# Kernel tuning notes

Hardware: AMD Instinct MI355X
Metric: run time of the kernel (lower is better)

## Reference

```python
import jax, jax.numpy as jnp
import numpy as np

N_ITER = 100
EPS = 1e-12


def _corr(x, k):
    # x: [C,H,W], k: [kh,kw]; per-channel 'same' cross-correlation, zero padding
    C = x.shape[0]
    kern = jnp.broadcast_to(k, (C, 1) + k.shape)
    return jax.lax.conv_general_dilated(
        x[None], kern, window_strides=(1, 1), padding='SAME',
        feature_group_count=C,
        dimension_numbers=('NCHW', 'OIHW', 'NCHW'))[0]


def _corr_t(x, k):
    # adjoint of zero-padded 'same' correlation = correlation with flipped kernel
    return _corr(x, k[::-1, ::-1])


def _A(x, kernel, reg_kernels, w2):
    # A x = K^T K x + sum_i w_i^2 R_i^T R_i x
    out = _corr_t(_corr(x, kernel), kernel)
    for i in range(reg_kernels.shape[0]):  # small fixed number of reg kernels
        rk = reg_kernels[i]
        out = out + w2[i] * _corr_t(_corr(x, rk), rk)
    return out


def setup_inputs() -> dict:
    key = jax.random.key(0)
    k1, k2, k3, k4 = jax.random.split(key, 4)
    image = jax.random.uniform(k1, (3, 768, 768), dtype=jnp.float32)
    kernel = jax.random.uniform(k2, (15, 15), dtype=jnp.float32)
    kernel = kernel / jnp.sum(kernel)  # normalized blur PSF
    reg_kernels = jax.random.normal(k3, (2, 5, 5), dtype=jnp.float32)
    reg_kernel_weights = jax.random.uniform(
        k4, (2,), dtype=jnp.float32, minval=1e-6, maxval=1.0)
    return {'image': image, 'kernel': kernel, 'reg_kernels': reg_kernels,
            'reg_kernel_weights': reg_kernel_weights}


def reference(image, kernel, reg_kernels, reg_kernel_weights):
    w2 = reg_kernel_weights ** 2
    # CG init: x0 = image, b = image, solve A x = K^T b
    KTb = _corr_t(image, kernel)
    r0 = KTb - _A(image, kernel, reg_kernels, w2)
    xrp0 = jnp.stack([image, r0, r0])  # [3, C, H, W]: x, r, p

    def body(xrp, _):
        x, r, p = xrp[0], xrp[1], xrp[2]
        Ap = _A(p, kernel, reg_kernels, w2)
        rtr = jnp.sum(r * r, axis=(1, 2), keepdims=True)      # per-channel [C,1,1]
        ptAp = jnp.sum(p * Ap, axis=(1, 2), keepdims=True)
        alpha = rtr / (ptAp + EPS)
        x_new = x + alpha * p
        r_new = r - alpha * Ap
        beta = jnp.sum(r_new * r_new, axis=(1, 2), keepdims=True) / (rtr + EPS)
        p_new = r_new + beta * p
        return jnp.stack([x_new, r_new, p_new]), None

    xrp, _ = jax.lax.scan(jax.checkpoint(body), xrp0, None, length=N_ITER)
    return xrp
```

## Files before the change

### kernel.cpp

```cpp
#include <hip/hip_runtime.h>

#define EPS 1e-12f

constexpr int H = 768, W = 768, C = 3;
constexpr int HW = H * W;
constexpr int CHW = C * HW;

constexpr int NSLOT = 16;
constexpr int SSTR = 16;
constexpr int SCALSZ = NSLOT * SSTR;

constexpr int SPW = 100, SPH = 60;
constexpr int S0W = 84;
constexpr int S1W = 76, S1H = 36;
constexpr int UBUF = SPH * SPW;
constexpr int LDSE = UBUF + 2 * S1H * S1W;
constexpr int IPW = 92, IPH = 60;

__device__ __forceinline__ float block_reduce_256(float v, float* redbuf) {
    #pragma unroll
    for (int off = 32; off > 0; off >>= 1) v += __shfl_down(v, off, 64);
    const int tid = threadIdx.x;
    if ((tid & 63) == 0) redbuf[tid >> 6] = v;
    __syncthreads();
    return redbuf[0] + redbuf[1] + redbuf[2] + redbuf[3];
}

__device__ __forceinline__ float sum_slots(const float* base, int c) {
    float s = 0.f;
    #pragma unroll
    for (int k = 0; k < NSLOT; ++k) s += base[k * SSTR + c];
    return s;
}

__global__ void tap_prep_k(const float* __restrict__ k15, const float* __restrict__ rks,
                           const float* __restrict__ rw, float* __restrict__ taps) {
    const int tid = threadIdx.x;
    if (tid < 240) {
        const int i = tid >> 4, j = tid & 15;
        taps[tid]       = (j < 15) ? k15[i * 15 + j] : 0.f;
        taps[240 + tid] = (j < 15) ? k15[(14 - i) * 15 + (14 - j)] : 0.f;
    }
    if (tid < 80) {
        const int kk = tid / 40, rem = tid % 40, i = rem >> 3, j = rem & 7;
        taps[480 + tid] = (j < 5) ? rks[kk * 25 + i * 5 + j] : 0.f;
        taps[560 + tid] = (j < 5) ? rks[kk * 25 + (4 - i) * 5 + (4 - j)] : 0.f;
    }
    const float w20 = rw[0] * rw[0], w21 = rw[1] * rw[1];
    if (tid == 0) { taps[1684] = w20; taps[1685] = w21; }
    for (int t = tid; t < 29 * 36; t += 256) {
        const int uy = t / 36, ux = t - uy * 36;
        float s = 0.f;
        if (ux < 29) {
            const int dy = uy - 14, dx = ux - 14;
            for (int sy = 0; sy < 15; ++sy) {
                const int ty = sy + dy;
                if ((unsigned)ty >= 15u) continue;
                for (int sx = 0; sx < 15; ++sx) {
                    const int tx = sx + dx;
                    if ((unsigned)tx < 15u) s += k15[sy * 15 + sx] * k15[ty * 15 + tx];
                }
            }
            if (dy >= -4 && dy <= 4 && dx >= -4 && dx <= 4) {
                float q0 = 0.f, q1 = 0.f;
                for (int sy = 0; sy < 5; ++sy) {
                    const int ty = sy + dy;
                    if ((unsigned)ty >= 5u) continue;
                    for (int sx = 0; sx < 5; ++sx) {
                        const int tx = sx + dx;
                        if ((unsigned)tx >= 5u) continue;
                        q0 += rks[sy * 5 + sx] * rks[ty * 5 + tx];
                        q1 += rks[25 + sy * 5 + sx] * rks[25 + ty * 5 + tx];
                    }
                }
                s += w20 * q0 + w21 * q1;
            }
        }
        taps[640 + t] = s;
    }
}

__global__ __launch_bounds__(256) void prologue_k(
    const float* __restrict__ img, const float* __restrict__ taps,
    float* __restrict__ outR, float* __restrict__ outP, float* __restrict__ outX,
    float* __restrict__ red)
{
    __shared__ __align__(16) float ub[UBUF];
    __shared__ __align__(16) float st1[S1H * S1W];
    __shared__ __align__(16) float st2[S1H * S1W];
    __shared__ float redbuf[4];

    const float* kt   = taps;
    const float* ktf  = taps + 240;
    const float* rkt  = taps + 480;
    const float* rktf = taps + 560;
    const float w02 = taps[1684], w12 = taps[1685];

    const int c = blockIdx.z;
    const int bx = blockIdx.x * 64, by = blockIdx.y * 32;
    const int tid = threadIdx.x;
    const float* inC = img + c * HW;

    for (int t = tid; t < SPH * 96; t += 256) {
        const int ly = t / 96, lx = t - ly * 96;
        const int gy = by - 14 + ly, gx = bx - 14 + lx;
        float v = 0.f;
        if ((unsigned)gy < (unsigned)H && (unsigned)gx < (unsigned)W) v = inC[gy * W + gx];
        ub[ly * SPW + lx] = v;
    }
    __syncthreads();

    const int oy = tid >> 3;
    const int ox = (tid & 7) << 3;

    {
        const int s0 = tid, s1i = tid + 256;
        const int row0 = s0 / 9, c0 = (s0 - row0 * 9) << 3;
        const int row1 = s1i / 9, c1 = (s1i - row1 * 9) << 3;
        const bool v1 = (s1i < 324);
        float b0[8], c0a[8], b1[8], c1a[8];
        #pragma unroll
        for (int k = 0; k < 8; ++k) { b0[k] = 0.f; c0a[k] = 0.f; b1[k] = 0.f; c1a[k] = 0.f; }
        #pragma unroll 1
        for (int i = 0; i < 5; ++i) {
            float kb[8], kc[8];
            #pragma unroll
            for (int q = 0; q < 2; ++q) {
                *(float4*)(kb + 4 * q) = *(const float4*)(rkt + i * 8 + 4 * q);
                *(float4*)(kc + 4 * q) = *(const float4*)(rkt + 40 + i * 8 + 4 * q);
            }
            {
                const float* rp = ub + (row0 + 10 + i) * SPW + c0 + 8;
                float seg[16];
                #pragma unroll
                for (int q = 0; q < 4; ++q) *(float4*)(seg + 4 * q) = *(const float4*)(rp + 4 * q);
                #pragma unroll
                for (int j = 0; j < 5; ++j)
                    #pragma unroll
                    for (int k = 0; k < 8; ++k) {
                        b0[k]  = fmaf(seg[j + k + 2], kb[j], b0[k]);
                        c0a[k] = fmaf(seg[j + k + 2], kc[j], c0a[k]);
                    }
            }
            if (v1) {
                const float* rp = ub + (row1 + 10 + i) * SPW + c1 + 8;
                float seg[16];
                #pragma unroll
                for (int q = 0; q < 4; ++q) *(float4*)(seg + 4 * q) = *(const float4*)(rp + 4 * q);
                #pragma unroll
                for (int j = 0; j < 5; ++j)
                    #pragma unroll
                    for (int k = 0; k < 8; ++k) {
                        b1[k]  = fmaf(seg[j + k + 2], kb[j], b1[k]);
                        c1a[k] = fmaf(seg[j + k + 2], kc[j], c1a[k]);
                    }
            }
        }
        {
            const int gy = by - 2 + row0, gxb = bx - 2 + c0;
            #pragma unroll
            for (int k = 0; k < 8; ++k)
                if (((unsigned)gy >= (unsigned)H) || ((unsigned)(gxb + k) >= (unsigned)W)) { b0[k] = 0.f; c0a[k] = 0.f; }
            float* o1 = st1 + row0 * S1W + c0;
            float* o2 = st2 + row0 * S1W + c0;
            *(float4*)(o1) = make_float4(b0[0], b0[1], b0[2], b0[3]);
            *(float4*)(o1 + 4) = make_float4(b0[4], b0[5], b0[6], b0[7]);
            *(float4*)(o2) = make_float4(c0a[0], c0a[1], c0a[2], c0a[3]);
            *(float4*)(o2 + 4) = make_float4(c0a[4], c0a[5], c0a[6], c0a[7]);
        }
        if (v1) {
            const int gy = by - 2 + row1, gxb = bx - 2 + c1;
            #pragma unroll
            for (int k = 0; k < 8; ++k)
                if (((unsigned)gy >= (unsigned)H) || ((unsigned)(gxb + k) >= (unsigned)W)) { b1[k] = 0.f; c1a[k] = 0.f; }
            float* o1 = st1 + row1 * S1W + c1;
            float* o2 = st2 + row1 * S1W + c1;
            *(float4*)(o1) = make_float4(b1[0], b1[1], b1[2], b1[3]);
            *(float4*)(o1 + 4) = make_float4(b1[4], b1[5], b1[6], b1[7]);
            *(float4*)(o2) = make_float4(c1a[0], c1a[1], c1a[2], c1a[3]);
            *(float4*)(o2 + 4) = make_float4(c1a[4], c1a[5], c1a[6], c1a[7]);
        }
    }

    float pctr[8];
    {
        const float* ctr = ub + (oy + 14) * SPW + ox + 14;
        #pragma unroll
        for (int k = 0; k < 8; ++k) pctr[k] = ctr[k];
    }

    float vimg[8];
    #pragma unroll
    for (int k = 0; k < 8; ++k) vimg[k] = 0.f;
    #pragma unroll 1
    for (int i = 0; i < 15; ++i) {
        const float* rowp = ub + (oy + 7 + i) * SPW + ox + 4;
        float seg[28];
        #pragma unroll
        for (int q = 0; q < 7; ++q) *(float4*)(seg + 4 * q) = *(const float4*)(rowp + 4 * q);
        float kv[16];
        #pragma unroll
        for (int q = 0; q < 4; ++q) *(float4*)(kv + 4 * q) = *(const float4*)(ktf + i * 16 + 4 * q);
        #pragma unroll
        for (int j = 0; j < 15; ++j)
            #pragma unroll
            for (int k = 0; k < 8; ++k) vimg[k] = fmaf(seg[j + k + 3], kv[j], vimg[k]);
    }

    const int s0 = tid, s1i = tid + 256;
    const int row0 = s0 / 10, ca0 = (s0 - row0 * 10) << 3;
    const int row1 = s1i / 10, ca1 = (s1i - row1 * 10) << 3;
    const bool av1 = (s1i < 460);
    float a0[8], a1[8];
    #pragma unroll
    for (int k = 0; k < 8; ++k) { a0[k] = 0.f; a1[k] = 0.f; }
    #pragma unroll 1
    for (int i = 0; i < 15; ++i) {
        float kv[16];
        #pragma unroll
        for (int q = 0; q < 4; ++q) *(float4*)(kv + 4 * q) = *(const float4*)(kt + i * 16 + 4 * q);
        {
            const float* rp = ub + (row0 + i) * SPW + ca0;
            float seg[24];
            #pragma unroll
            for (int q = 0; q < 6; ++q) *(float4*)(seg + 4 * q) = *(const float4*)(rp + 4 * q);
            #pragma unroll
            for (int j = 0; j < 15; ++j)
                #pragma unroll
                for (int k = 0; k < 8; ++k) a0[k] = fmaf(seg[j + k], kv[j], a0[k]);
        }
        if (av1) {
            const float* rp = ub + (row1 + i) * SPW + ca1;
            float seg[24];
            #pragma unroll
            for (int q = 0; q < 6; ++q) *(float4*)(seg + 4 * q) = *(const float4*)(rp + 4 * q);
            #pragma unroll
            for (int j = 0; j < 15; ++j)
                #pragma unroll
                for (int k = 0; k < 8; ++k) a1[k] = fmaf(seg[j + k], kv[j], a1[k]);
        }
    }
    {
        const int gy = by - 7 + row0, gxb = bx - 7 + ca0;
        #pragma unroll
        for (int k = 0; k < 8; ++k)
            if (((unsigned)gy >= (unsigned)H) || ((unsigned)(gxb + k) >= (unsigned)W)) a0[k] = 0.f;
    }
    if (av1) {
        const int gy = by - 7 + row1, gxb = bx - 7 + ca1;
        #pragma unroll
        for (int k = 0; k < 8; ++k)
            if (((unsigned)gy >= (unsigned)H) || ((unsigned)(gxb + k) >= (unsigned)W)) a1[k] = 0.f;
    }
    __syncthreads();
    {
        float* o = ub + row0 * S0W + ca0;
        *(float4*)(o) = make_float4(a0[0], a0[1], a0[2], a0[3]);
        *(float4*)(o + 4) = make_float4(a0[4], a0[5], a0[6], a0[7]);
    }
    if (av1) {
        float* o = ub + row1 * S0W + ca1;
        *(float4*)(o) = make_float4(a1[0], a1[1], a1[2], a1[3]);
        *(float4*)(o + 4) = make_float4(a1[4], a1[5], a1[6], a1[7]);
    }
    __syncthreads();

    float acc[8];
    #pragma unroll
    for (int k = 0; k < 8; ++k) acc[k] = 0.f;
    #pragma unroll 1
    for (int i = 0; i < 15; ++i) {
        float kv[16];
        #pragma unroll
        for (int q = 0; q < 4; ++q) *(float4*)(kv + 4 * q) = *(const float4*)(ktf + i * 16 + 4 * q);
        const float* rp = ub + (oy + i) * S0W + ox;
        float seg[24];
        #pragma unroll
        for (int q = 0; q < 6; ++q) *(float4*)(seg + 4 * q) = *(const float4*)(rp + 4 * q);
        #pragma unroll
        for (int j = 0; j < 15; ++j)
            #pragma unroll
            for (int k = 0; k < 8; ++k) acc[k] = fmaf(seg[j + k], kv[j], acc[k]);
    }
    float accB[8], accC[8];
    #pragma unroll
    for (int k = 0; k < 8; ++k) { accB[k] = 0.f; accC[k] = 0.f; }
    #pragma unroll 1
    for (int i = 0; i < 5; ++i) {
        float kb[8], kc[8];
        #pragma unroll
        for (int q = 0; q < 2; ++q) {
            *(float4*)(kb + 4 * q) = *(const float4*)(rktf + i * 8 + 4 * q);
            *(float4*)(kc + 4 * q) = *(const float4*)(rktf + 40 + i * 8 + 4 * q);
        }
        const float* r1p = st1 + (oy + i) * S1W + ox;
        const float* r2p = st2 + (oy + i) * S1W + ox;
        float sA[12], sB[12];
        #pragma unroll
        for (int q = 0; q < 3; ++q) *(float4*)(sA + 4 * q) = *(const float4*)(r1p + 4 * q);
        #pragma unroll
        for (int q = 0; q < 3; ++q) *(float4*)(sB + 4 * q) = *(const float4*)(r2p + 4 * q);
        #pragma unroll
        for (int j = 0; j < 5; ++j)
            #pragma unroll
            for (int k = 0; k < 8; ++k) {
                accB[k] = fmaf(sA[j + k], kb[j], accB[k]);
                accC[k] = fmaf(sB[j + k], kc[j], accC[k]);
            }
    }

    float v[8];
    #pragma unroll
    for (int k = 0; k < 8; ++k) v[k] = vimg[k] - (acc[k] + w02 * accB[k] + w12 * accC[k]);

    const int g = c * HW + (by + oy) * W + bx + ox;
    *(float4*)(outR + g)     = make_float4(v[0], v[1], v[2], v[3]);
    *(float4*)(outR + g + 4) = make_float4(v[4], v[5], v[6], v[7]);
    *(float4*)(outP + g)     = make_float4(v[0], v[1], v[2], v[3]);
    *(float4*)(outP + g + 4) = make_float4(v[4], v[5], v[6], v[7]);
    *(float4*)(outX + g)     = make_float4(pctr[0], pctr[1], pctr[2], pctr[3]);
    *(float4*)(outX + g + 4) = make_float4(pctr[4], pctr[5], pctr[6], pctr[7]);
    float local = 0.f;
    #pragma unroll
    for (int k = 0; k < 8; ++k) local += v[k] * v[k];
    const float tot = block_reduce_256(local, redbuf);
    if (tid == 0) {
        const int bid = blockIdx.y * gridDim.x + blockIdx.x;
        atomicAdd(red + (bid & (NSLOT - 1)) * SSTR + c, tot);
    }
}

template <bool FIRST>
__global__ __launch_bounds__(256) void stepA_k(
    const float* __restrict__ pold, const float* __restrict__ rvec,
    float* __restrict__ x, const float* __restrict__ taps,
    float* __restrict__ Apnew, float* __restrict__ pnew,
    const float* __restrict__ rtrI, const float* __restrict__ rtrIm1,
    const float* __restrict__ ptapIm1, float* __restrict__ ptapI)
{
    __shared__ __align__(16) float lds[LDSE];
    __shared__ float redbuf[4];
    const int c = blockIdx.z;
    const int tid = threadIdx.x;
    const int bid = blockIdx.x;

    float alpha = 0.f, beta = 0.f;
    if (!FIRST) {
        const float ri   = sum_slots(rtrI, c);
        const float rim1 = sum_slots(rtrIm1, c);
        const float ptm1 = sum_slots(ptapIm1, c);
        beta  = ri / (rim1 + EPS);
        alpha = rim1 / (ptm1 + EPS);
    }

    float S1 = 0.f;

    if (bid < 68) {
        float* ub  = lds;
        float* st1 = lds + UBUF;
        float* st2 = st1 + S1H * S1W;
        const float* kt   = taps;
        const float* ktf  = taps + 240;
        const float* rkt  = taps + 480;
        const float* rktf = taps + 560;
        const float w02 = taps[1684], w12 = taps[1685];

        int tbx, tby;
        { const int e = bid;
          if (e < 12)      { tbx = e;      tby = 0; }
          else if (e < 24) { tbx = e - 12; tby = 23; }
          else if (e < 46) { tbx = 0;      tby = 1 + (e - 24); }
          else             { tbx = 11;     tby = 1 + (e - 46); } }
        const int bx = tbx * 64, by = tby * 32;

        for (int s = tid; s < SPH * 96; s += 256) {
            const int ly = s / 96, lx = s - ly * 96;
            const int gy = by - 14 + ly, gx = bx - 14 + lx;
            float pe = 0.f;
            if ((unsigned)gy < (unsigned)H && (unsigned)gx < (unsigned)W) {
                const int g = c * HW + gy * W + gx;
                const float pv = pold[g];
                if (FIRST) pe = pv;
                else {
                    pe = fmaf(beta, pv, rvec[g]);
                    if (ly >= 14 && ly < 46 && lx >= 14 && lx < 78) {
                        pnew[g] = pe;
                        x[g] = fmaf(alpha, pv, x[g]);
                    }
                }
            }
            ub[ly * SPW + lx] = pe;
        }
        __syncthreads();

        const int oy = tid >> 3;
        const int ox = (tid & 7) << 3;

        {
            const int s0 = tid, s1i = tid + 256;
            const int row0 = s0 / 9, c0 = (s0 - row0 * 9) << 3;
            const int row1 = s1i / 9, c1 = (s1i - row1 * 9) << 3;
            const bool v1 = (s1i < 324);
            float b0[8], c0a[8], b1[8], c1a[8];
            #pragma unroll
            for (int k = 0; k < 8; ++k) { b0[k] = 0.f; c0a[k] = 0.f; b1[k] = 0.f; c1a[k] = 0.f; }
            #pragma unroll 1
            for (int i = 0; i < 5; ++i) {
                float kb[8], kc[8];
                #pragma unroll
                for (int q = 0; q < 2; ++q) {
                    *(float4*)(kb + 4 * q) = *(const float4*)(rkt + i * 8 + 4 * q);
                    *(float4*)(kc + 4 * q) = *(const float4*)(rkt + 40 + i * 8 + 4 * q);
                }
                {
                    const float* rp = ub + (row0 + 10 + i) * SPW + c0 + 8;
                    float seg[16];
                    #pragma unroll
                    for (int q = 0; q < 4; ++q) *(float4*)(seg + 4 * q) = *(const float4*)(rp + 4 * q);
                    #pragma unroll
                    for (int j = 0; j < 5; ++j)
                        #pragma unroll
                        for (int k = 0; k < 8; ++k) {
                            b0[k]  = fmaf(seg[j + k + 2], kb[j], b0[k]);
                            c0a[k] = fmaf(seg[j + k + 2], kc[j], c0a[k]);
                        }
                }
                if (v1) {
                    const float* rp = ub + (row1 + 10 + i) * SPW + c1 + 8;
                    float seg[16];
                    #pragma unroll
                    for (int q = 0; q < 4; ++q) *(float4*)(seg + 4 * q) = *(const float4*)(rp + 4 * q);
                    #pragma unroll
                    for (int j = 0; j < 5; ++j)
                        #pragma unroll
                        for (int k = 0; k < 8; ++k) {
                            b1[k]  = fmaf(seg[j + k + 2], kb[j], b1[k]);
                            c1a[k] = fmaf(seg[j + k + 2], kc[j], c1a[k]);
                        }
                }
            }
            {
                const int gy = by - 2 + row0, gxb = bx - 2 + c0;
                #pragma unroll
                for (int k = 0; k < 8; ++k)
                    if (((unsigned)gy >= (unsigned)H) || ((unsigned)(gxb + k) >= (unsigned)W)) { b0[k] = 0.f; c0a[k] = 0.f; }
                float* o1 = st1 + row0 * S1W + c0;
                float* o2 = st2 + row0 * S1W + c0;
                *(float4*)(o1) = make_float4(b0[0], b0[1], b0[2], b0[3]);
                *(float4*)(o1 + 4) = make_float4(b0[4], b0[5], b0[6], b0[7]);
                *(float4*)(o2) = make_float4(c0a[0], c0a[1], c0a[2], c0a[3]);
                *(float4*)(o2 + 4) = make_float4(c0a[4], c0a[5], c0a[6], c0a[7]);
            }
            if (v1) {
                const int gy = by - 2 + row1, gxb = bx - 2 + c1;
                #pragma unroll
                for (int k = 0; k < 8; ++k)
                    if (((unsigned)gy >= (unsigned)H) || ((unsigned)(gxb + k) >= (unsigned)W)) { b1[k] = 0.f; c1a[k] = 0.f; }
                float* o1 = st1 + row1 * S1W + c1;
                float* o2 = st2 + row1 * S1W + c1;
                *(float4*)(o1) = make_float4(b1[0], b1[1], b1[2], b1[3]);
                *(float4*)(o1 + 4) = make_float4(b1[4], b1[5], b1[6], b1[7]);
                *(float4*)(o2) = make_float4(c1a[0], c1a[1], c1a[2], c1a[3]);
                *(float4*)(o2 + 4) = make_float4(c1a[4], c1a[5], c1a[6], c1a[7]);
            }
        }

        float pctr[8];
        {
            const float* ctr = ub + (oy + 14) * SPW + ox + 14;
            #pragma unroll
            for (int k = 0; k < 8; ++k) pctr[k] = ctr[k];
        }

        const int s0 = tid, s1i = tid + 256;
        const int row0 = s0 / 10, ca0 = (s0 - row0 * 10) << 3;
        const int row1 = s1i / 10, ca1 = (s1i - row1 * 10) << 3;
        const bool av1 = (s1i < 460);
        float a0[8], a1[8];
        #pragma unroll
        for (int k = 0; k < 8; ++k) { a0[k] = 0.f; a1[k] = 0.f; }
        #pragma unroll 1
        for (int i = 0; i < 15; ++i) {
            float kv[16];
            #pragma unroll
            for (int q = 0; q < 4; ++q) *(float4*)(kv + 4 * q) = *(const float4*)(kt + i * 16 + 4 * q);
            {
                const float* rp = ub + (row0 + i) * SPW + ca0;
                float seg[24];
                #pragma unroll
                for (int q = 0; q < 6; ++q) *(float4*)(seg + 4 * q) = *(const float4*)(rp + 4 * q);
                #pragma unroll
                for (int j = 0; j < 15; ++j)
                    #pragma unroll
                    for (int k = 0; k < 8; ++k) a0[k] = fmaf(seg[j + k], kv[j], a0[k]);
            }
            if (av1) {
                const float* rp = ub + (row1 + i) * SPW + ca1;
                float seg[24];
                #pragma unroll
                for (int q = 0; q < 6; ++q) *(float4*)(seg + 4 * q) = *(const float4*)(rp + 4 * q);
                #pragma unroll
                for (int j = 0; j < 15; ++j)
                    #pragma unroll
                    for (int k = 0; k < 8; ++k) a1[k] = fmaf(seg[j + k], kv[j], a1[k]);
            }
        }
        {
            const int gy = by - 7 + row0, gxb = bx - 7 + ca0;
            #pragma unroll
            for (int k = 0; k < 8; ++k)
                if (((unsigned)gy >= (unsigned)H) || ((unsigned)(gxb + k) >= (unsigned)W)) a0[k] = 0.f;
        }
        if (av1) {
            const int gy = by - 7 + row1, gxb = bx - 7 + ca1;
            #pragma unroll
            for (int k = 0; k < 8; ++k)
                if (((unsigned)gy >= (unsigned)H) || ((unsigned)(gxb + k) >= (unsigned)W)) a1[k] = 0.f;
        }
        __syncthreads();
        {
            float* o = ub + row0 * S0W + ca0;
            *(float4*)(o) = make_float4(a0[0], a0[1], a0[2], a0[3]);
            *(float4*)(o + 4) = make_float4(a0[4], a0[5], a0[6], a0[7]);
        }
        if (av1) {
            float* o = ub + row1 * S0W + ca1;
            *(float4*)(o) = make_float4(a1[0], a1[1], a1[2], a1[3]);
            *(float4*)(o + 4) = make_float4(a1[4], a1[5], a1[6], a1[7]);
        }
        __syncthreads();

        float acc[8];
        #pragma unroll
        for (int k = 0; k < 8; ++k) acc[k] = 0.f;
        #pragma unroll 1
        for (int i = 0; i < 15; ++i) {
            float kv[16];
            #pragma unroll
            for (int q = 0; q < 4; ++q) *(float4*)(kv + 4 * q) = *(const float4*)(ktf + i * 16 + 4 * q);
            const float* rp = ub + (oy + i) * S0W + ox;
            float seg[24];
            #pragma unroll
            for (int q = 0; q < 6; ++q) *(float4*)(seg + 4 * q) = *(const float4*)(rp + 4 * q);
            #pragma unroll
            for (int j = 0; j < 15; ++j)
                #pragma unroll
                for (int k = 0; k < 8; ++k) acc[k] = fmaf(seg[j + k], kv[j], acc[k]);
        }
        float accB[8], accC[8];
        #pragma unroll
        for (int k = 0; k < 8; ++k) { accB[k] = 0.f; accC[k] = 0.f; }
        #pragma unroll 1
        for (int i = 0; i < 5; ++i) {
            float kb[8], kc[8];
            #pragma unroll
            for (int q = 0; q < 2; ++q) {
                *(float4*)(kb + 4 * q) = *(const float4*)(rktf + i * 8 + 4 * q);
                *(float4*)(kc + 4 * q) = *(const float4*)(rktf + 40 + i * 8 + 4 * q);
            }
            const float* r1p = st1 + (oy + i) * S1W + ox;
            const float* r2p = st2 + (oy + i) * S1W + ox;
            float sA[12], sB[12];
            #pragma unroll
            for (int q = 0; q < 3; ++q) *(float4*)(sA + 4 * q) = *(const float4*)(r1p + 4 * q);
            #pragma unroll
            for (int q = 0; q < 3; ++q) *(float4*)(sB + 4 * q) = *(const float4*)(r2p + 4 * q);
            #pragma unroll
            for (int j = 0; j < 5; ++j)
                #pragma unroll
                for (int k = 0; k < 8; ++k) {
                    accB[k] = fmaf(sA[j + k], kb[j], accB[k]);
                    accC[k] = fmaf(sB[j + k], kc[j], accC[k]);
                }
        }

        float v[8];
        #pragma unroll
        for (int k = 0; k < 8; ++k) v[k] = acc[k] + w02 * accB[k] + w12 * accC[k];

        const int g = c * HW + (by + oy) * W + bx + ox;
        *(float4*)(Apnew + g)     = make_float4(v[0], v[1], v[2], v[3]);
        *(float4*)(Apnew + g + 4) = make_float4(v[4], v[5], v[6], v[7]);
        #pragma unroll
        for (int k = 0; k < 8; ++k) S1 += pctr[k] * v[k];
    } else {
        const float* tk = taps + 640;
        const int b = bid - 68;
        const int bx = 64 + (b % 10) * 64, by = 32 + (b / 10) * 32;
        const int gy0 = by - 14, gx0 = bx - 14;

        for (int s = tid; s < IPH * IPW; s += 256) {
            const int ly = s / IPW, lx = s - ly * IPW;
            const int g = c * HW + (gy0 + ly) * W + (gx0 + lx);
            const float pv = pold[g];
            float pe;
            if (FIRST) pe = pv;
            else {
                pe = fmaf(beta, pv, rvec[g]);
                if (ly >= 14 && ly < 46 && lx >= 14 && lx < 78) {
                    pnew[g] = pe;
                    x[g] = fmaf(alpha, pv, x[g]);
                }
            }
            lds[s] = pe;
        }
        __syncthreads();

        const int ox = (tid & 15) << 2;
        const int o0 = (tid >> 4) << 1;

        float a0[4], a1[4];
        #pragma unroll
        for (int k = 0; k < 4; ++k) { a0[k] = 0.f; a1[k] = 0.f; }
        {
            const float* rp = lds + o0 * IPW + ox;
            float seg[32];
            #pragma unroll
            for (int q = 0; q < 8; ++q) *(float4*)(seg + 4 * q) = *(const float4*)(rp + 4 * q);
            #pragma unroll
            for (int j = 0; j < 29; ++j) {
                const float kv = tk[j];
                #pragma unroll
                for (int k = 0; k < 4; ++k) a0[k] = fmaf(seg[j + k], kv, a0[k]);
            }
        }
        #pragma unroll 1
        for (int d = 1; d <= 28; ++d) {
            const float* rp = lds + (o0 + d) * IPW + ox;
            float seg[32];
            #pragma unroll
            for (int q = 0; q < 8; ++q) *(float4*)(seg + 4 * q) = *(const float4*)(rp + 4 * q);
            const float* kr0 = tk + d * 36;
            const float* kr1 = kr0 - 36;
            #pragma unroll
            for (int j = 0; j < 29; ++j) {
                const float kv0 = kr0[j], kv1 = kr1[j];
                #pragma unroll
                for (int k = 0; k < 4; ++k) {
                    a0[k] = fmaf(seg[j + k], kv0, a0[k]);
                    a1[k] = fmaf(seg[j + k], kv1, a1[k]);
                }
            }
        }
        {
            const float* rp = lds + (o0 + 29) * IPW + ox;
            float seg[32];
            #pragma unroll
            for (int q = 0; q < 8; ++q) *(float4*)(seg + 4 * q) = *(const float4*)(rp + 4 * q);
            const float* kr1 = tk + 28 * 36;
            #pragma unroll
            for (int j = 0; j < 29; ++j) {
                const float kv = kr1[j];
                #pragma unroll
                for (int k = 0; k < 4; ++k) a1[k] = fmaf(seg[j + k], kv, a1[k]);
            }
        }

        const int gbase = c * HW + (by + o0) * W + bx + ox;
        const float* c0p = lds + (o0 + 14) * IPW + ox + 14;
        const float* c1p = c0p + IPW;
        *(float4*)(Apnew + gbase)     = make_float4(a0[0], a0[1], a0[2], a0[3]);
        *(float4*)(Apnew + gbase + W) = make_float4(a1[0], a1[1], a1[2], a1[3]);
        #pragma unroll
        for (int k = 0; k < 4; ++k) S1 += c0p[k] * a0[k] + c1p[k] * a1[k];
    }

    const float tot = block_reduce_256(S1, redbuf);
    if (tid == 0) atomicAdd(ptapI + (bid & (NSLOT - 1)) * SSTR + c, tot);
}

__global__ __launch_bounds__(256) void cgr_k(
    float* __restrict__ r, const float* __restrict__ Ap,
    const float* __restrict__ rtrI, const float* __restrict__ ptapI,
    float* __restrict__ rtrNext)
{
    __shared__ float redbuf[4];
    const int c = blockIdx.z;
    const float alpha = sum_slots(rtrI, c) / (sum_slots(ptapI, c) + EPS);
    const int idx = c * HW + (blockIdx.x * 256 + threadIdx.x) * 8;
    float local = 0.f;
    #pragma unroll
    for (int h = 0; h < 2; ++h) {
        const int o = idx + 4 * h;
        float4 rv = *(float4*)(r + o);
        const float4 av = *(const float4*)(Ap + o);
        rv.x = fmaf(-alpha, av.x, rv.x);
        rv.y = fmaf(-alpha, av.y, rv.y);
        rv.z = fmaf(-alpha, av.z, rv.z);
        rv.w = fmaf(-alpha, av.w, rv.w);
        *(float4*)(r + o) = rv;
        local += rv.x * rv.x + rv.y * rv.y + rv.z * rv.z + rv.w * rv.w;
    }
    const float tot = block_reduce_256(local, redbuf);
    if (threadIdx.x == 0)
        atomicAdd(rtrNext + ((int)blockIdx.x & (NSLOT - 1)) * SSTR + c, tot);
}

__global__ __launch_bounds__(256) void ep_k(
    float* __restrict__ x, const float* __restrict__ r100, const float* __restrict__ p99,
    float* __restrict__ pout,
    const float* __restrict__ rtr99s, const float* __restrict__ rtr100s,
    const float* __restrict__ ptap99s)
{
    const int c = blockIdx.z;
    const float rtr99 = sum_slots(rtr99s, c);
    const float alpha = rtr99 / (sum_slots(ptap99s, c) + EPS);
    const float beta  = sum_slots(rtr100s, c) / (rtr99 + EPS);
    const int idx = c * HW + (blockIdx.x * 256 + threadIdx.x) * 8;
    #pragma unroll
    for (int h = 0; h < 2; ++h) {
        const int o = idx + 4 * h;
        const float4 pv = *(const float4*)(p99 + o);
        const float4 rv = *(const float4*)(r100 + o);
        float4 xv = *(float4*)(x + o);
        xv.x = fmaf(alpha, pv.x, xv.x); xv.y = fmaf(alpha, pv.y, xv.y);
        xv.z = fmaf(alpha, pv.z, xv.z); xv.w = fmaf(alpha, pv.w, xv.w);
        *(float4*)(x + o) = xv;
        *(float4*)(pout + o) = make_float4(
            fmaf(beta, pv.x, rv.x), fmaf(beta, pv.y, rv.y),
            fmaf(beta, pv.z, rv.z), fmaf(beta, pv.w, rv.w));
    }
}

extern "C" void kernel_launch(void* const* d_in, const int* in_sizes, int n_in,
                              void* d_out, int out_size, void* d_ws, size_t ws_size,
                              hipStream_t stream)
{
    const float* img = (const float*)d_in[0];
    const float* k15 = (const float*)d_in[1];
    const float* rks = (const float*)d_in[2];
    const float* rw  = (const float*)d_in[3];

    float* out = (float*)d_out;
    float* xs = out;
    float* rs = out + CHW;
    float* ps = out + 2 * CHW;

    float* ws = (float*)d_ws;
    float* pA   = ws;
    float* pB   = ws + CHW;
    float* Ap   = ws + 2 * CHW;
    float* scal = ws + 3 * CHW;
    float* rtrS  = scal;
    float* ptapS = scal + 101 * SCALSZ;
    float* taps  = scal + 201 * SCALSZ;

    float* pbuf[2] = { pA, pB };

    hipMemsetAsync(scal, 0, (size_t)201 * SCALSZ * sizeof(float), stream);
    tap_prep_k<<<1, 256, 0, stream>>>(k15, rks, rw, taps);

    const dim3 bc(256);
    prologue_k<<<dim3(12, 24, 3), bc, 0, stream>>>(img, taps, rs, pA, xs, rtrS);

    for (int i = 0; i < 100; ++i) {
        if (i == 0) {
            stepA_k<true><<<dim3(288, 1, 3), bc, 0, stream>>>(
                pA, rs, xs, taps, Ap, nullptr,
                rtrS, rtrS, ptapS, ptapS);
        } else {
            stepA_k<false><<<dim3(288, 1, 3), bc, 0, stream>>>(
                pbuf[(i - 1) & 1], rs, xs, taps, Ap, pbuf[i & 1],
                rtrS + (size_t)i * SCALSZ, rtrS + (size_t)(i - 1) * SCALSZ,
                ptapS + (size_t)(i - 1) * SCALSZ, ptapS + (size_t)i * SCALSZ);
        }
        cgr_k<<<dim3(288, 1, 3), bc, 0, stream>>>(
            rs, Ap, rtrS + (size_t)i * SCALSZ, ptapS + (size_t)i * SCALSZ,
            rtrS + (size_t)(i + 1) * SCALSZ);
    }
    ep_k<<<dim3(288, 1, 3), bc, 0, stream>>>(
        xs, rs, pB, ps,
        rtrS + (size_t)99 * SCALSZ, rtrS + (size_t)100 * SCALSZ,
        ptapS + (size_t)99 * SCALSZ);
}
```

Measured before the change: 8.744 ms.

## Split edge tiles into half-height blocks and move x update into residual kernel

Border tiles of the fused A·p kernel are split into two 16-row halves, so there are 136 edge blocks instead of 68, each with a smaller LDS footprint and 4 outputs per thread. This is meant to rebalance the slow padded edge blocks against the interior blocks. The x += alpha·p update moves from stepA (where it ran against the previous p) into cgr_k using the current p, which removes the alpha computation from stepA but adds an extra read and write stream to cgr_k. Splitting the edge tiles also recomputes more halo per block.

```diff
diff --git a/kernel.cpp b/kernel.cpp
--- a/kernel.cpp
+++ b/kernel.cpp
@@ -14,8 +14,13 @@
 constexpr int S0W = 84;
 constexpr int S1W = 76, S1H = 36;
 constexpr int UBUF = SPH * SPW;
-constexpr int LDSE = UBUF + 2 * S1H * S1W;
+
+constexpr int ESPH = 44;
+constexpr int ET0H = 30;
+constexpr int ES1H = 20;
+constexpr int ELDS = ESPH * SPW + 2 * ES1H * S1W;
 constexpr int IPW = 92, IPH = 60;
+constexpr int NEDGE = 136;
 
 __device__ __forceinline__ float block_reduce_256(float v, float* redbuf) {
     #pragma unroll
@@ -333,47 +338,41 @@
 template <bool FIRST>
 __global__ __launch_bounds__(256) void stepA_k(
     const float* __restrict__ pold, const float* __restrict__ rvec,
-    float* __restrict__ x, const float* __restrict__ taps,
+    const float* __restrict__ taps,
     float* __restrict__ Apnew, float* __restrict__ pnew,
     const float* __restrict__ rtrI, const float* __restrict__ rtrIm1,
-    const float* __restrict__ ptapIm1, float* __restrict__ ptapI)
+    float* __restrict__ ptapI)
 {
-    __shared__ __align__(16) float lds[LDSE];
+    __shared__ __align__(16) float lds[ELDS];
     __shared__ float redbuf[4];
     const int c = blockIdx.z;
     const int tid = threadIdx.x;
     const int bid = blockIdx.x;
 
-    float alpha = 0.f, beta = 0.f;
-    if (!FIRST) {
-        const float ri   = sum_slots(rtrI, c);
-        const float rim1 = sum_slots(rtrIm1, c);
-        const float ptm1 = sum_slots(ptapIm1, c);
-        beta  = ri / (rim1 + EPS);
-        alpha = rim1 / (ptm1 + EPS);
-    }
+    float beta = 0.f;
+    if (!FIRST) beta = sum_slots(rtrI, c) / (sum_slots(rtrIm1, c) + EPS);
 
     float S1 = 0.f;
 
-    if (bid < 68) {
+    if (bid < NEDGE) {
         float* ub  = lds;
-        float* st1 = lds + UBUF;
-        float* st2 = st1 + S1H * S1W;
+        float* st1 = lds + ESPH * SPW;
+        float* st2 = st1 + ES1H * S1W;
         const float* kt   = taps;
         const float* ktf  = taps + 240;
         const float* rkt  = taps + 480;
         const float* rktf = taps + 560;
         const float w02 = taps[1684], w12 = taps[1685];
 
+        const int e = bid >> 1, half = bid & 1;
         int tbx, tby;
-        { const int e = bid;
-          if (e < 12)      { tbx = e;      tby = 0; }
+        { if (e < 12)      { tbx = e;      tby = 0; }
           else if (e < 24) { tbx = e - 12; tby = 23; }
           else if (e < 46) { tbx = 0;      tby = 1 + (e - 24); }
           else             { tbx = 11;     tby = 1 + (e - 46); } }
-        const int bx = tbx * 64, by = tby * 32;
-
-        for (int s = tid; s < SPH * 96; s += 256) {
+        const int bx = tbx * 64, by = tby * 32 + half * 16;
+
+        for (int s = tid; s < ESPH * 96; s += 256) {
             const int ly = s / 96, lx = s - ly * 96;
             const int gy = by - 14 + ly, gx = bx - 14 + lx;
             float pe = 0.f;
@@ -383,36 +382,31 @@
                 if (FIRST) pe = pv;
                 else {
                     pe = fmaf(beta, pv, rvec[g]);
-                    if (ly >= 14 && ly < 46 && lx >= 14 && lx < 78) {
-                        pnew[g] = pe;
-                        x[g] = fmaf(alpha, pv, x[g]);
+                    if (ly >= 14 && ly < 30 && lx >= 14 && lx < 78) pnew[g] = pe;
+                }
+            }
+            ub[ly * SPW + lx] = pe;
+        }
+        __syncthreads();
+
+        const int oy2 = tid >> 4;
+        const int ox2 = (tid & 15) << 2;
+
+        {
+            const int row0 = tid / 9, c0 = (tid - (tid / 9) * 9) << 3;
+            const bool act = (tid < 180);
+            float b0[8], c0a[8];
+            #pragma unroll
+            for (int k = 0; k < 8; ++k) { b0[k] = 0.f; c0a[k] = 0.f; }
+            if (act) {
+                #pragma unroll 1
+                for (int i = 0; i < 5; ++i) {
+                    float kb[8], kc[8];
+                    #pragma unroll
+                    for (int q = 0; q < 2; ++q) {
+                        *(float4*)(kb + 4 * q) = *(const float4*)(rkt + i * 8 + 4 * q);
+                        *(float4*)(kc + 4 * q) = *(const float4*)(rkt + 40 + i * 8 + 4 * q);
                     }
-                }
-            }
-            ub[ly * SPW + lx] = pe;
-        }
-        __syncthreads();
-
-        const int oy = tid >> 3;
-        const int ox = (tid & 7) << 3;
-
-        {
-            const int s0 = tid, s1i = tid + 256;
-            const int row0 = s0 / 9, c0 = (s0 - row0 * 9) << 3;
-            const int row1 = s1i / 9, c1 = (s1i - row1 * 9) << 3;
-            const bool v1 = (s1i < 324);
-            float b0[8], c0a[8], b1[8], c1a[8];
-            #pragma unroll
-            for (int k = 0; k < 8; ++k) { b0[k] = 0.f; c0a[k] = 0.f; b1[k] = 0.f; c1a[k] = 0.f; }
-            #pragma unroll 1
-            for (int i = 0; i < 5; ++i) {
-                float kb[8], kc[8];
-                #pragma unroll
-                for (int q = 0; q < 2; ++q) {
-                    *(float4*)(kb + 4 * q) = *(const float4*)(rkt + i * 8 + 4 * q);
-                    *(float4*)(kc + 4 * q) = *(const float4*)(rkt + 40 + i * 8 + 4 * q);
-                }
-                {
                     const float* rp = ub + (row0 + 10 + i) * SPW + c0 + 8;
                     float seg[16];
                     #pragma unroll
@@ -425,21 +419,6 @@
                             c0a[k] = fmaf(seg[j + k + 2], kc[j], c0a[k]);
                         }
                 }
-                if (v1) {
-                    const float* rp = ub + (row1 + 10 + i) * SPW + c1 + 8;
-                    float seg[16];
-                    #pragma unroll
-                    for (int q = 0; q < 4; ++q) *(float4*)(seg + 4 * q) = *(const float4*)(rp + 4 * q);
-                    #pragma unroll
-                    for (int j = 0; j < 5; ++j)
-                        #pragma unroll
-                        for (int k = 0; k < 8; ++k) {
-                            b1[k]  = fmaf(seg[j + k + 2], kb[j], b1[k]);
-                            c1a[k] = fmaf(seg[j + k + 2], kc[j], c1a[k]);
-                        }
-                }
-            }
-            {
                 const int gy = by - 2 + row0, gxb = bx - 2 + c0;
                 #pragma unroll
                 for (int k = 0; k < 8; ++k)
@@ -451,31 +430,19 @@
                 *(float4*)(o2) = make_float4(c0a[0], c0a[1], c0a[2], c0a[3]);
                 *(float4*)(o2 + 4) = make_float4(c0a[4], c0a[5], c0a[6], c0a[7]);
             }
-            if (v1) {
-                const int gy = by - 2 + row1, gxb = bx - 2 + c1;
-                #pragma unroll
-                for (int k = 0; k < 8; ++k)
-                    if (((unsigned)gy >= (unsigned)H) || ((unsigned)(gxb + k) >= (unsigned)W)) { b1[k] = 0.f; c1a[k] = 0.f; }
-                float* o1 = st1 + row1 * S1W + c1;
-                float* o2 = st2 + row1 * S1W + c1;
-                *(float4*)(o1) = make_float4(b1[0], b1[1], b1[2], b1[3]);
-                *(float4*)(o1 + 4) = make_float4(b1[4], b1[5], b1[6], b1[7]);
-                *(float4*)(o2) = make_float4(c1a[0], c1a[1], c1a[2], c1a[3]);
-                *(float4*)(o2 + 4) = make_float4(c1a[4], c1a[5], c1a[6], c1a[7]);
-            }
-        }
-
-        float pctr[8];
+        }
+
+        float pctr[4];
         {
-            const float* ctr = ub + (oy + 14) * SPW + ox + 14;
-            #pragma unroll
-            for (int k = 0; k < 8; ++k) pctr[k] = ctr[k];
+            const float* ctr = ub + (oy2 + 14) * SPW + ox2 + 14;
+            #pragma unroll
+            for (int k = 0; k < 4; ++k) pctr[k] = ctr[k];
         }
 
         const int s0 = tid, s1i = tid + 256;
         const int row0 = s0 / 10, ca0 = (s0 - row0 * 10) << 3;
         const int row1 = s1i / 10, ca1 = (s1i - row1 * 10) << 3;
-        const bool av1 = (s1i < 460);
+        const bool av1 = (s1i < 300);
         float a0[8], a1[8];
         #pragma unroll
         for (int k = 0; k < 8; ++k) { a0[k] = 0.f; a1[k] = 0.f; }
@@ -530,26 +497,26 @@
         }
         __syncthreads();
 
-        float acc[8];
-        #pragma unroll
-        for (int k = 0; k < 8; ++k) acc[k] = 0.f;
+        float acc[4];
+        #pragma unroll
+        for (int k = 0; k < 4; ++k) acc[k] = 0.f;
         #pragma unroll 1
         for (int i = 0; i < 15; ++i) {
             float kv[16];
             #pragma unroll
             for (int q = 0; q < 4; ++q) *(float4*)(kv + 4 * q) = *(const float4*)(ktf + i * 16 + 4 * q);
-            const float* rp = ub + (oy + i) * S0W + ox;
-            float seg[24];
-            #pragma unroll
-            for (int q = 0; q < 6; ++q) *(float4*)(seg + 4 * q) = *(const float4*)(rp + 4 * q);
+            const float* rp = ub + (oy2 + i) * S0W + ox2;
+            float seg[20];
+            #pragma unroll
+            for (int q = 0; q < 5; ++q) *(float4*)(seg + 4 * q) = *(const float4*)(rp + 4 * q);
             #pragma unroll
             for (int j = 0; j < 15; ++j)
                 #pragma unroll
-                for (int k = 0; k < 8; ++k) acc[k] = fmaf(seg[j + k], kv[j], acc[k]);
-        }
-        float accB[8], accC[8];
-        #pragma unroll
-        for (int k = 0; k < 8; ++k) { accB[k] = 0.f; accC[k] = 0.f; }
+                for (int k = 0; k < 4; ++k) acc[k] = fmaf(seg[j + k], kv[j], acc[k]);
+        }
+        float accB[4], accC[4];
+        #pragma unroll
+        for (int k = 0; k < 4; ++k) { accB[k] = 0.f; accC[k] = 0.f; }
         #pragma unroll 1
         for (int i = 0; i < 5; ++i) {
             float kb[8], kc[8];
@@ -558,34 +525,33 @@
                 *(float4*)(kb + 4 * q) = *(const float4*)(rktf + i * 8 + 4 * q);
                 *(float4*)(kc + 4 * q) = *(const float4*)(rktf + 40 + i * 8 + 4 * q);
             }
-            const float* r1p = st1 + (oy + i) * S1W + ox;
-            const float* r2p = st2 + (oy + i) * S1W + ox;
-            float sA[12], sB[12];
-            #pragma unroll
-            for (int q = 0; q < 3; ++q) *(float4*)(sA + 4 * q) = *(const float4*)(r1p + 4 * q);
-            #pragma unroll
-            for (int q = 0; q < 3; ++q) *(float4*)(sB + 4 * q) = *(const float4*)(r2p + 4 * q);
+            const float* r1p = st1 + (oy2 + i) * S1W + ox2;
+            const float* r2p = st2 + (oy2 + i) * S1W + ox2;
+            float sA[8], sB[8];
+            #pragma unroll
+            for (int q = 0; q < 2; ++q) *(float4*)(sA + 4 * q) = *(const float4*)(r1p + 4 * q);
+            #pragma unroll
+            for (int q = 0; q < 2; ++q) *(float4*)(sB + 4 * q) = *(const float4*)(r2p + 4 * q);
             #pragma unroll
             for (int j = 0; j < 5; ++j)
                 #pragma unroll
-                for (int k = 0; k < 8; ++k) {
+                for (int k = 0; k < 4; ++k) {
                     accB[k] = fmaf(sA[j + k], kb[j], accB[k]);
                     accC[k] = fmaf(sB[j + k], kc[j], accC[k]);
                 }
         }
 
-        float v[8];
-        #pragma unroll
-        for (int k = 0; k < 8; ++k) v[k] = acc[k] + w02 * accB[k] + w12 * accC[k];
-
-        const int g = c * HW + (by + oy) * W + bx + ox;
-        *(float4*)(Apnew + g)     = make_float4(v[0], v[1], v[2], v[3]);
-        *(float4*)(Apnew + g + 4) = make_float4(v[4], v[5], v[6], v[7]);
-        #pragma unroll
-        for (int k = 0; k < 8; ++k) S1 += pctr[k] * v[k];
+        float v[4];
+        #pragma unroll
+        for (int k = 0; k < 4; ++k) v[k] = acc[k] + w02 * accB[k] + w12 * accC[k];
+
+        const int g = c * HW + (by + oy2) * W + bx + ox2;
+        *(float4*)(Apnew + g) = make_float4(v[0], v[1], v[2], v[3]);
+        #pragma unroll
+        for (int k = 0; k < 4; ++k) S1 += pctr[k] * v[k];
     } else {
         const float* tk = taps + 640;
-        const int b = bid - 68;
+        const int b = bid - NEDGE;
         const int bx = 64 + (b % 10) * 64, by = 32 + (b / 10) * 32;
         const int gy0 = by - 14, gx0 = bx - 14;
 
@@ -597,10 +563,7 @@
             if (FIRST) pe = pv;
             else {
                 pe = fmaf(beta, pv, rvec[g]);
-                if (ly >= 14 && ly < 46 && lx >= 14 && lx < 78) {
-                    pnew[g] = pe;
-                    x[g] = fmaf(alpha, pv, x[g]);
-                }
+                if (ly >= 14 && ly < 46 && lx >= 14 && lx < 78) pnew[g] = pe;
             }
             lds[s] = pe;
         }
@@ -671,6 +634,7 @@
 
 __global__ __launch_bounds__(256) void cgr_k(
     float* __restrict__ r, const float* __restrict__ Ap,
+    float* __restrict__ x, const float* __restrict__ p,
     const float* __restrict__ rtrI, const float* __restrict__ ptapI,
     float* __restrict__ rtrNext)
 {
@@ -683,12 +647,15 @@
     for (int h = 0; h < 2; ++h) {
         const int o = idx + 4 * h;
         float4 rv = *(float4*)(r + o);
+        float4 xv = *(float4*)(x + o);
         const float4 av = *(const float4*)(Ap + o);
-        rv.x = fmaf(-alpha, av.x, rv.x);
-        rv.y = fmaf(-alpha, av.y, rv.y);
-        rv.z = fmaf(-alpha, av.z, rv.z);
-        rv.w = fmaf(-alpha, av.w, rv.w);
+        const float4 pv = *(const float4*)(p + o);
+        rv.x = fmaf(-alpha, av.x, rv.x); xv.x = fmaf(alpha, pv.x, xv.x);
+        rv.y = fmaf(-alpha, av.y, rv.y); xv.y = fmaf(alpha, pv.y, xv.y);
+        rv.z = fmaf(-alpha, av.z, rv.z); xv.z = fmaf(alpha, pv.z, xv.z);
+        rv.w = fmaf(-alpha, av.w, rv.w); xv.w = fmaf(alpha, pv.w, xv.w);
         *(float4*)(r + o) = rv;
+        *(float4*)(x + o) = xv;
         local += rv.x * rv.x + rv.y * rv.y + rv.z * rv.z + rv.w * rv.w;
     }
     const float tot = block_reduce_256(local, redbuf);
@@ -697,25 +664,17 @@
 }
 
 __global__ __launch_bounds__(256) void ep_k(
-    float* __restrict__ x, const float* __restrict__ r100, const float* __restrict__ p99,
-    float* __restrict__ pout,
-    const float* __restrict__ rtr99s, const float* __restrict__ rtr100s,
-    const float* __restrict__ ptap99s)
+    const float* __restrict__ r100, const float* __restrict__ p99, float* __restrict__ pout,
+    const float* __restrict__ rtr99s, const float* __restrict__ rtr100s)
 {
     const int c = blockIdx.z;
-    const float rtr99 = sum_slots(rtr99s, c);
-    const float alpha = rtr99 / (sum_slots(ptap99s, c) + EPS);
-    const float beta  = sum_slots(rtr100s, c) / (rtr99 + EPS);
+    const float beta = sum_slots(rtr100s, c) / (sum_slots(rtr99s, c) + EPS);
     const int idx = c * HW + (blockIdx.x * 256 + threadIdx.x) * 8;
     #pragma unroll
     for (int h = 0; h < 2; ++h) {
         const int o = idx + 4 * h;
         const float4 pv = *(const float4*)(p99 + o);
         const float4 rv = *(const float4*)(r100 + o);
-        float4 xv = *(float4*)(x + o);
-        xv.x = fmaf(alpha, pv.x, xv.x); xv.y = fmaf(alpha, pv.y, xv.y);
-        xv.z = fmaf(alpha, pv.z, xv.z); xv.w = fmaf(alpha, pv.w, xv.w);
-        *(float4*)(x + o) = xv;
         *(float4*)(pout + o) = make_float4(
             fmaf(beta, pv.x, rv.x), fmaf(beta, pv.y, rv.y),
             fmaf(beta, pv.z, rv.z), fmaf(beta, pv.w, rv.w));
@@ -754,22 +713,23 @@
     prologue_k<<<dim3(12, 24, 3), bc, 0, stream>>>(img, taps, rs, pA, xs, rtrS);
 
     for (int i = 0; i < 100; ++i) {
+        float* pcur;
         if (i == 0) {
-            stepA_k<true><<<dim3(288, 1, 3), bc, 0, stream>>>(
-                pA, rs, xs, taps, Ap, nullptr,
-                rtrS, rtrS, ptapS, ptapS);
+            pcur = pA;
+            stepA_k<true><<<dim3(NEDGE + 220, 1, 3), bc, 0, stream>>>(
+                pA, rs, taps, Ap, nullptr, rtrS, rtrS, ptapS);
         } else {
-            stepA_k<false><<<dim3(288, 1, 3), bc, 0, stream>>>(
-                pbuf[(i - 1) & 1], rs, xs, taps, Ap, pbuf[i & 1],
+            pcur = pbuf[i & 1];
+            stepA_k<false><<<dim3(NEDGE + 220, 1, 3), bc, 0, stream>>>(
+                pbuf[(i - 1) & 1], rs, taps, Ap, pcur,
                 rtrS + (size_t)i * SCALSZ, rtrS + (size_t)(i - 1) * SCALSZ,
-                ptapS + (size_t)(i - 1) * SCALSZ, ptapS + (size_t)i * SCALSZ);
+                ptapS + (size_t)i * SCALSZ);
         }
         cgr_k<<<dim3(288, 1, 3), bc, 0, stream>>>(
-            rs, Ap, rtrS + (size_t)i * SCALSZ, ptapS + (size_t)i * SCALSZ,
+            rs, Ap, xs, pcur,
+            rtrS + (size_t)i * SCALSZ, ptapS + (size_t)i * SCALSZ,
             rtrS + (size_t)(i + 1) * SCALSZ);
     }
     ep_k<<<dim3(288, 1, 3), bc, 0, stream>>>(
-        xs, rs, pB, ps,
-        rtrS + (size_t)99 * SCALSZ, rtrS + (size_t)100 * SCALSZ,
-        ptapS + (size_t)99 * SCALSZ);
+        rs, pB, ps, rtrS + (size_t)99 * SCALSZ, rtrS + (size_t)100 * SCALSZ);
 }
```

Measured after the change: 8.736 ms. No clear change (-0.1%).
